# Performance work log

Hardware: AMD Instinct MI355X
Metric: run time of the kernel (lower is better)

The kernel has to match this reference:

```python
import jax, jax.numpy as jnp
import numpy as np

B, T, C = 4, 2048, 1024
H = 16
D = C // H  # head_dim = 64

def setup_inputs() -> dict:
    key = jax.random.key(0)
    k1, k2, k3 = jax.random.split(key, 3)
    x = jax.random.normal(k1, (B, T, C), dtype=jnp.float32)
    w_qkv = jax.random.normal(k2, (C, 3 * C), dtype=jnp.float32) * (1.0 / np.sqrt(C))
    w_proj = jax.random.normal(k3, (C, C), dtype=jnp.float32) * (1.0 / np.sqrt(C))
    return {"x": x, "w_qkv": w_qkv, "w_proj": w_proj}

def reference(x, w_qkv, w_proj):
    Bq, Tq, Cq = x.shape
    qkv = x @ w_qkv                                   # [B,T,3C]
    q, k, v = jnp.split(qkv, 3, axis=2)
    # [B,T,C] -> [B,H,T,D]
    q = q.reshape(Bq, Tq, H, D).transpose(0, 2, 1, 3)
    k = k.reshape(Bq, Tq, H, D).transpose(0, 2, 1, 3)
    v = v.reshape(Bq, Tq, H, D).transpose(0, 2, 1, 3)
    att = jnp.einsum('bhqd,bhkd->bhqk', q, k) / jnp.sqrt(jnp.float32(D))
    causal = jnp.tril(jnp.ones((Tq, Tq), dtype=bool))
    att = jnp.where(causal[None, None], att, jnp.float32(-jnp.inf))
    att = jax.nn.softmax(att, axis=-1)
    y = jnp.einsum('bhqk,bhkd->bhqd', att, v)         # [B,H,T,D]
    y = y.transpose(0, 2, 1, 3).reshape(Bq, Tq, Cq)
    return y @ w_proj
```

## Files before the change

kernel.cpp:

```cpp
#include <hip/hip_runtime.h>

typedef unsigned short u16;
typedef __attribute__((ext_vector_type(8))) short s16x8;
typedef __attribute__((ext_vector_type(4))) float f32x4;
typedef __attribute__((ext_vector_type(16))) float f32x16;

#define MFMA(a, b, c) __builtin_amdgcn_mfma_f32_16x16x32_bf16((a), (b), (c), 0, 0, 0)
#define MFMA32(a, b, c) __builtin_amdgcn_mfma_f32_32x32x16_bf16((a), (b), (c), 0, 0, 0)

#define LDS16(gp, lp)                                                          \
  __builtin_amdgcn_global_load_lds(                                            \
      (__attribute__((address_space(1))) void*)(gp),                           \
      (__attribute__((address_space(3))) void*)(lp), 16, 0, 0)

#if __has_builtin(__builtin_amdgcn_exp2f)
#define EXP2F(x) __builtin_amdgcn_exp2f(x)
#else
#define EXP2F(x) exp2f(x)
#endif
#if __has_builtin(__builtin_amdgcn_rcpf)
#define RCPF(x) __builtin_amdgcn_rcpf(x)
#else
#define RCPF(x) (1.0f / (x))
#endif

__device__ __forceinline__ u16 f2bf(float f) {
  unsigned u = __float_as_uint(f);
  u += 0x7fffu + ((u >> 16) & 1u);
  return (u16)(u >> 16);
}

__device__ __forceinline__ int cvtpk(float a, float b) {
  int r;
  asm("v_cvt_pk_bf16_f32 %0, %1, %2" : "=v"(r) : "v"(a), "v"(b));
  return r;
}

__global__ void cast_x_kernel(const float* __restrict__ in, u16* __restrict__ out) {
  const int idx = (blockIdx.x * 256 + threadIdx.x) * 4;
  const float4 v = *(const float4*)(in + idx);
  ushort4 o;
  o.x = f2bf(v.x); o.y = f2bf(v.y); o.z = f2bf(v.z); o.w = f2bf(v.w);
  *(ushort4*)(out + idx) = o;
}

__global__ void transpose_cast(const float* __restrict__ in, u16* __restrict__ out,
                               int Kd, int Nd) {
  __shared__ float t[64][65];
  const int tid = threadIdx.x;
  const int nb = blockIdx.x * 64, kb = blockIdx.y * 64;
#pragma unroll
  for (int it = 0; it < 4; it++) {
    const int flat = it * 1024 + tid * 4;
    const int rr = flat >> 6, cc = flat & 63;
    const float4 v = *(const float4*)(in + (size_t)(kb + rr) * Nd + nb + cc);
    t[rr][cc] = v.x; t[rr][cc + 1] = v.y; t[rr][cc + 2] = v.z; t[rr][cc + 3] = v.w;
  }
  __syncthreads();
#pragma unroll
  for (int it = 0; it < 4; it++) {
    const int flat = it * 1024 + tid * 4;
    const int rn = flat >> 6, ck = flat & 63;
    ushort4 o;
    o.x = f2bf(t[ck][rn]);     o.y = f2bf(t[ck + 1][rn]);
    o.z = f2bf(t[ck + 2][rn]); o.w = f2bf(t[ck + 3][rn]);
    *(ushort4*)(out + (size_t)(nb + rn) * Kd + kb + ck) = o;
  }
}

template <int EPI>
__global__ __launch_bounds__(256, 2)
void gemm128(const u16* __restrict__ A, const u16* __restrict__ Bt,
             float* __restrict__ Cout, int Ndim,
             u16* __restrict__ qp, u16* __restrict__ kp, u16* __restrict__ vp) {
  __shared__ alignas(16) u16 As[128 * 32];
  __shared__ alignas(16) u16 Bs[128 * 32];
  const int tid = threadIdx.x;
  const int wave = tid >> 6, lane = tid & 63;
  const int r = lane & 15, qq = lane >> 4;
  const int wm = (wave >> 1) * 64, wn = (wave & 1) * 64;
  const int gx = gridDim.x;
  const int nwg = gx * gridDim.y;
  const int bid = blockIdx.x + gx * blockIdx.y;
  const int swz = (bid & 7) * (nwg >> 3) + (bid >> 3);
  const int tn = (swz % gx) * 128, tm = (swz / gx) * 128;

  f32x4 acc[4][4];
#pragma unroll
  for (int i = 0; i < 4; i++)
#pragma unroll
    for (int j = 0; j < 4; j++) acc[i][j] = (f32x4){0.f, 0.f, 0.f, 0.f};

  const int c0 = tid, c1 = tid + 256;
  const u16* ga0 = A + (size_t)(tm + (c0 >> 2)) * 1024 + (c0 & 3) * 8;
  const u16* ga1 = A + (size_t)(tm + (c1 >> 2)) * 1024 + (c1 & 3) * 8;
  const u16* gb0 = Bt + (size_t)(tn + (c0 >> 2)) * 1024 + (c0 & 3) * 8;
  const u16* gb1 = Bt + (size_t)(tn + (c1 >> 2)) * 1024 + (c1 & 3) * 8;
  u16* la0 = As + c0 * 8; u16* la1 = As + c1 * 8;
  u16* lb0 = Bs + c0 * 8; u16* lb1 = Bs + c1 * 8;

  for (int k0 = 0; k0 < 1024; k0 += 32) {
    LDS16(ga0 + k0, la0);
    LDS16(ga1 + k0, la1);
    LDS16(gb0 + k0, lb0);
    LDS16(gb1 + k0, lb1);
    __syncthreads();
    s16x8 af[4], bfr[4];
#pragma unroll
    for (int f = 0; f < 4; f++)
      af[f] = *(const s16x8*)(As + (wm + f * 16 + r) * 32 + qq * 8);
#pragma unroll
    for (int f = 0; f < 4; f++)
      bfr[f] = *(const s16x8*)(Bs + (wn + f * 16 + r) * 32 + qq * 8);
    __builtin_amdgcn_s_setprio(1);
#pragma unroll
    for (int fm = 0; fm < 4; fm++)
#pragma unroll
      for (int fn = 0; fn < 4; fn++)
        acc[fm][fn] = MFMA(af[fm], bfr[fn], acc[fm][fn]);
    __builtin_amdgcn_s_setprio(0);
    __syncthreads();
  }

  if (EPI == 0) {
#pragma unroll
    for (int fm = 0; fm < 4; fm++) {
#pragma unroll
      for (int j2 = 0; j2 < 4; j2++) {
        const int mm = tm + wm + fm * 16 + qq * 4 + j2;
        const int bb = mm >> 11, tt = mm & 2047;
#pragma unroll
        for (int fn = 0; fn < 4; fn++) {
          const int n = tn + wn + fn * 16 + r;
          const u16 bv = f2bf(acc[fm][fn][j2]);
          const int which = n >> 10;
          const int hh = (n >> 6) & 15, dd = n & 63;
          const int bhh = bb * 16 + hh;
          if (which == 0)      qp[((size_t)bhh * 2048 + tt) * 64 + dd] = bv;
          else if (which == 1) kp[((size_t)bhh * 2048 + tt) * 64 + dd] = bv;
          else                 vp[((size_t)bhh * 64 + dd) * 2048 + tt] = bv;
        }
      }
    }
  } else {
#pragma unroll
    for (int fm = 0; fm < 4; fm++) {
#pragma unroll
      for (int j2 = 0; j2 < 4; j2++) {
        const int mm = tm + wm + fm * 16 + qq * 4 + j2;
#pragma unroll
        for (int fn = 0; fn < 4; fn++) {
          const int n = tn + wn + fn * 16 + r;
          Cout[(size_t)mm * Ndim + n] = acc[fm][fn][j2];
        }
      }
    }
  }
}

__global__ __launch_bounds__(256, 2)
void attn_fwd(const u16* __restrict__ qg, const u16* __restrict__ kg,
              const u16* __restrict__ vtg, u16* __restrict__ yg) {
  __shared__ alignas(16) u16 Kl[2][64 * 64];
  __shared__ alignas(16) u16 Vl[2][64 * 64];
  const int tid = threadIdx.x;
  const int w = tid >> 6, lane = tid & 63;
  const int q5 = lane & 31, hi = lane >> 5;
  const int bh = blockIdx.x;
  const int qi = (int)(gridDim.y - 1 - blockIdx.y);
  const int qb = qi * 128;
  const int qrow = qb + w * 32 + q5;
  const float C = 0.18033688011112042f;

  const u16* qbase = qg + ((size_t)bh * 2048 + qrow) * 64;
  s16x8 qf[4];
#pragma unroll
  for (int ks = 0; ks < 4; ks++)
    qf[ks] = *(const s16x8*)(qbase + ks * 16 + hi * 8);

  const int c0 = tid, c1 = tid + 256;
  const int r0 = c0 >> 3, s0 = (c0 & 7) ^ (r0 & 7);
  const int r1 = c1 >> 3, s1 = (c1 & 7) ^ (r1 & 7);
  const u16* kga = kg + ((size_t)bh * 2048 + r0) * 64 + s0 * 8;
  const u16* kgb = kg + ((size_t)bh * 2048 + r1) * 64 + s1 * 8;
  const u16* vga = vtg + ((size_t)bh * 64 + r0) * 2048 + s0 * 8;
  const u16* vgb = vtg + ((size_t)bh * 64 + r1) * 2048 + s1 * 8;

  f32x16 ya, yb;
#pragma unroll
  for (int r = 0; r < 16; r++) { ya[r] = 0.f; yb[r] = 0.f; }
  float m_run = -3.0e38f, l_run = 0.f;

  const int nt = qb / 64 + 2;

#define STAGE(b, t)                                               \
  do {                                                            \
    LDS16(kga + (size_t)(t) * 4096, Kl[b] + c0 * 8);              \
    LDS16(kgb + (size_t)(t) * 4096, Kl[b] + c1 * 8);              \
    LDS16(vga + (size_t)(t) * 64,   Vl[b] + c0 * 8);              \
    LDS16(vgb + (size_t)(t) * 64,   Vl[b] + c1 * 8);              \
  } while (0)

  STAGE(0, 0);
  __syncthreads();

  for (int t = 0; t < nt; t++) {
    const int buf = t & 1;
    if (t + 1 < nt) STAGE(buf ^ 1, t + 1);
    const int kv0 = t * 64;
    const u16* Kb = Kl[buf];
    const u16* Vb = Vl[buf];

    if (kv0 <= qb + w * 32 + 31) {
      f32x16 sa, sb;
#pragma unroll
      for (int r = 0; r < 16; r++) { sa[r] = 0.f; sb[r] = 0.f; }
      __builtin_amdgcn_s_setprio(1);
#pragma unroll
      for (int ks = 0; ks < 4; ks++) {
        const int slot = ((ks * 2 + hi) ^ (lane & 7)) * 8;
        const s16x8 ka  = *(const s16x8*)(Kb + q5 * 64 + slot);
        const s16x8 kb2 = *(const s16x8*)(Kb + (32 + q5) * 64 + slot);
        sa = MFMA32(ka, qf[ks], sa);
        sb = MFMA32(kb2, qf[ks], sb);
      }
      __builtin_amdgcn_s_setprio(0);

      s16x8 va[4], vb2[4];
#pragma unroll
      for (int ks4 = 0; ks4 < 4; ks4++) {
        const int sv = ((ks4 * 2 + hi) ^ (lane & 7)) * 8;
        va[ks4]  = *(const s16x8*)(Vb + q5 * 64 + sv);
        vb2[ks4] = *(const s16x8*)(Vb + (32 + q5) * 64 + sv);
      }

      if (kv0 + 63 > qb + w * 32) {
#pragma unroll
        for (int r = 0; r < 16; r++) {
          const int kl = kv0 + (r & 3) + 8 * (r >> 2) + 4 * hi;
          if (kl > qrow)      sa[r] = -3.0e38f;
          if (kl + 32 > qrow) sb[r] = -3.0e38f;
        }
      }

      float mx0 = -3.0e38f, mx1 = -3.0e38f, mx2 = -3.0e38f, mx3 = -3.0e38f;
#pragma unroll
      for (int r = 0; r < 16; r += 4) {
        mx0 = fmaxf(mx0, fmaxf(sa[r], sb[r]));
        mx1 = fmaxf(mx1, fmaxf(sa[r + 1], sb[r + 1]));
        mx2 = fmaxf(mx2, fmaxf(sa[r + 2], sb[r + 2]));
        mx3 = fmaxf(mx3, fmaxf(sa[r + 3], sb[r + 3]));
      }
      float mx = fmaxf(fmaxf(mx0, mx1), fmaxf(mx2, mx3));
      mx = fmaxf(mx, __shfl_xor(mx, 32));
      const float mxs = mx * C;

      if (!__all(mxs - m_run <= 8.0f)) {
        const float m2 = fmaxf(m_run, mxs);
        const float alpha = EXP2F(m_run - m2);
        m_run = m2;
        l_run *= alpha;
#pragma unroll
        for (int r = 0; r < 16; r++) { ya[r] *= alpha; yb[r] *= alpha; }
      }

      const float nm2 = -m_run;
      float ls0 = 0.f, ls1 = 0.f, ls2 = 0.f, ls3 = 0.f;
#pragma unroll
      for (int r = 0; r < 16; r += 4) {
        float p;
        p = EXP2F(fmaf(sa[r], C, nm2));     sa[r] = p;     ls0 += p;
        p = EXP2F(fmaf(sa[r + 1], C, nm2)); sa[r + 1] = p; ls1 += p;
        p = EXP2F(fmaf(sa[r + 2], C, nm2)); sa[r + 2] = p; ls2 += p;
        p = EXP2F(fmaf(sa[r + 3], C, nm2)); sa[r + 3] = p; ls3 += p;
        p = EXP2F(fmaf(sb[r], C, nm2));     sb[r] = p;     ls0 += p;
        p = EXP2F(fmaf(sb[r + 1], C, nm2)); sb[r + 1] = p; ls1 += p;
        p = EXP2F(fmaf(sb[r + 2], C, nm2)); sb[r + 2] = p; ls2 += p;
        p = EXP2F(fmaf(sb[r + 3], C, nm2)); sb[r + 3] = p; ls3 += p;
      }
      float ls = (ls0 + ls1) + (ls2 + ls3);
      ls += __shfl_xor(ls, 32);
      l_run += ls;

      s16x8 bfrag[4];
#pragma unroll
      for (int kb = 0; kb < 2; kb++) {
        const f32x16* pv = kb ? &sb : &sa;
        int wv[8], xv[8];
#pragma unroll
        for (int i = 0; i < 8; i++) wv[i] = cvtpk((*pv)[2 * i], (*pv)[2 * i + 1]);
#pragma unroll
        for (int i = 0; i < 8; i++) xv[i] = __shfl_xor(wv[i], 32);
        union { int4 i4; s16x8 s8; } u0, u1;
        u0.i4 = hi ? make_int4(xv[2], xv[3], wv[2], wv[3])
                   : make_int4(wv[0], wv[1], xv[0], xv[1]);
        u1.i4 = hi ? make_int4(xv[6], xv[7], wv[6], wv[7])
                   : make_int4(wv[4], wv[5], xv[4], xv[5]);
        bfrag[kb * 2]     = u0.s8;
        bfrag[kb * 2 + 1] = u1.s8;
      }

      __builtin_amdgcn_s_setprio(1);
#pragma unroll
      for (int ks4 = 0; ks4 < 4; ks4++) {
        ya = MFMA32(va[ks4], bfrag[ks4], ya);
        yb = MFMA32(vb2[ks4], bfrag[ks4], yb);
      }
      __builtin_amdgcn_s_setprio(0);
    }
    __syncthreads();
  }
#undef STAGE

  const float linv = RCPF(l_run);
  const int b = bh >> 4, h = bh & 15;
  u16* yrow = yg + ((size_t)b * 2048 + qrow) * 1024 + h * 64;
#pragma unroll
  for (int dt = 0; dt < 2; dt++) {
    const f32x16* Y = dt ? &yb : &ya;
#pragma unroll
    for (int p2 = 0; p2 < 8; p2++) {
      const int pk = cvtpk((*Y)[2 * p2] * linv, (*Y)[2 * p2 + 1] * linv);
      const int d0 = dt * 32 + (p2 >> 1) * 8 + hi * 4 + (p2 & 1) * 2;
      *reinterpret_cast<int*>(yrow + d0) = pk;
    }
  }
}

extern "C" void kernel_launch(void* const* d_in, const int* in_sizes, int n_in,
                              void* d_out, int out_size, void* d_ws, size_t ws_size,
                              hipStream_t stream) {
  const float* x = (const float*)d_in[0];
  const float* wqkv = (const float*)d_in[1];
  const float* wproj = (const float*)d_in[2];
  float* out = (float*)d_out;

  char* ws = (char*)d_ws;
  u16* xb     = (u16*)(ws);
  u16* wqkvT  = (u16*)(ws + 16777216);
  u16* wprojT = (u16*)(ws + 23068672);
  u16* qw     = (u16*)(ws + 25165824);
  u16* kw     = (u16*)(ws + 41943040);
  u16* vtw    = (u16*)(ws + 58720256);
  u16* yw     = (u16*)(ws + 75497472);
  (void)in_sizes; (void)n_in; (void)out_size; (void)ws_size;

  cast_x_kernel<<<8192, 256, 0, stream>>>(x, xb);
  transpose_cast<<<dim3(48, 16), 256, 0, stream>>>(wqkv, wqkvT, 1024, 3072);
  transpose_cast<<<dim3(16, 16), 256, 0, stream>>>(wproj, wprojT, 1024, 1024);
  gemm128<0><<<dim3(24, 64), 256, 0, stream>>>(xb, wqkvT, nullptr, 3072, qw, kw, vtw);
  attn_fwd<<<dim3(64, 16), 256, 0, stream>>>(qw, kw, vtw, yw);
  gemm128<1><<<dim3(8, 64), 256, 0, stream>>>(yw, wprojT, out, 1024,
                                              nullptr, nullptr, nullptr);
}
```

Baseline: 269.8 us.

## Pipeline GEMM with 4-stage LDS ring and 256x128 tiles using 512 threads

Replaces the single-buffered 128x128 GEMM with a 256x128 tile computed by 8 waves. The K-loop now streams into a 4-slot LDS ring, issuing global-to-LDS loads three stages ahead and using vmcnt waits plus one barrier per step. This hides global load latency and removes the second barrier per iteration. In exchange it uses more LDS per block (96KB) and adds a k-major LDS layout that may cause bank conflicts.

```diff
diff --git a/kernel.cpp b/kernel.cpp
--- a/kernel.cpp
+++ b/kernel.cpp
@@ -12,6 +12,8 @@
   __builtin_amdgcn_global_load_lds(                                            \
       (__attribute__((address_space(1))) void*)(gp),                           \
       (__attribute__((address_space(3))) void*)(lp), 16, 0, 0)
+
+#define WAITVM(n) asm volatile("s_waitcnt vmcnt(" #n ")" ::: "memory")
 
 #if __has_builtin(__builtin_amdgcn_exp2f)
 #define EXP2F(x) __builtin_amdgcn_exp2f(x)
@@ -69,21 +71,20 @@
 }
 
 template <int EPI>
-__global__ __launch_bounds__(256, 2)
-void gemm128(const u16* __restrict__ A, const u16* __restrict__ Bt,
+__global__ __launch_bounds__(512, 2)
+void gemm256(const u16* __restrict__ A, const u16* __restrict__ Bt,
              float* __restrict__ Cout, int Ndim,
              u16* __restrict__ qp, u16* __restrict__ kp, u16* __restrict__ vp) {
-  __shared__ alignas(16) u16 As[128 * 32];
-  __shared__ alignas(16) u16 Bs[128 * 32];
+  __shared__ alignas(16) u16 L[4 * 12288];
   const int tid = threadIdx.x;
-  const int wave = tid >> 6, lane = tid & 63;
+  const int lane = tid & 63, wid = tid >> 6;
   const int r = lane & 15, qq = lane >> 4;
-  const int wm = (wave >> 1) * 64, wn = (wave & 1) * 64;
+  const int wr = wid >> 1, wc = wid & 1;
   const int gx = gridDim.x;
   const int nwg = gx * gridDim.y;
   const int bid = blockIdx.x + gx * blockIdx.y;
   const int swz = (bid & 7) * (nwg >> 3) + (bid >> 3);
-  const int tn = (swz % gx) * 128, tm = (swz / gx) * 128;
+  const int tn = (swz % gx) * 128, tm = (swz / gx) * 256;
 
   f32x4 acc[4][4];
 #pragma unroll
@@ -91,47 +92,70 @@
 #pragma unroll
     for (int j = 0; j < 4; j++) acc[i][j] = (f32x4){0.f, 0.f, 0.f, 0.f};
 
-  const int c0 = tid, c1 = tid + 256;
-  const u16* ga0 = A + (size_t)(tm + (c0 >> 2)) * 1024 + (c0 & 3) * 8;
-  const u16* ga1 = A + (size_t)(tm + (c1 >> 2)) * 1024 + (c1 & 3) * 8;
-  const u16* gb0 = Bt + (size_t)(tn + (c0 >> 2)) * 1024 + (c0 & 3) * 8;
-  const u16* gb1 = Bt + (size_t)(tn + (c1 >> 2)) * 1024 + (c1 & 3) * 8;
-  u16* la0 = As + c0 * 8; u16* la1 = As + c1 * 8;
-  u16* lb0 = Bs + c0 * 8; u16* lb1 = Bs + c1 * 8;
-
-  for (int k0 = 0; k0 < 1024; k0 += 32) {
-    LDS16(ga0 + k0, la0);
-    LDS16(ga1 + k0, la1);
-    LDS16(gb0 + k0, lb0);
-    LDS16(gb1 + k0, lb1);
-    __syncthreads();
-    s16x8 af[4], bfr[4];
-#pragma unroll
-    for (int f = 0; f < 4; f++)
-      af[f] = *(const s16x8*)(As + (wm + f * 16 + r) * 32 + qq * 8);
-#pragma unroll
-    for (int f = 0; f < 4; f++)
-      bfr[f] = *(const s16x8*)(Bs + (wn + f * 16 + r) * 32 + qq * 8);
-    __builtin_amdgcn_s_setprio(1);
-#pragma unroll
-    for (int fm = 0; fm < 4; fm++)
-#pragma unroll
-      for (int fn = 0; fn < 4; fn++)
-        acc[fm][fn] = MFMA(af[fm], bfr[fn], acc[fm][fn]);
-    __builtin_amdgcn_s_setprio(0);
-    __syncthreads();
-  }
+  const u16* gA = A + (size_t)(tm + (tid & 255)) * 1024 + (tid >> 8) * 8;
+  const u16* gB = Bt + (size_t)(tn + (tid & 127)) * 1024 + (tid >> 7) * 8;
+  const int la0 = tid * 8, la1 = (tid + 512) * 8, lb0 = 8192 + tid * 8;
+
+#define GSTAGE(b, t)                                                \
+  do {                                                              \
+    const u16* ga_ = gA + (t) * 32;                                 \
+    u16* lp_ = L + (b) * 12288;                                     \
+    LDS16(ga_, lp_ + la0);                                          \
+    LDS16(ga_ + 16, lp_ + la1);                                     \
+    LDS16(gB + (t) * 32, lp_ + lb0);                                \
+  } while (0)
+
+  const int arow = wr * 64 + r, brow = wc * 64 + r;
+  const int aoff = qq * 2048 + arow * 8;
+  const int boff = 8192 + qq * 1024 + brow * 8;
+
+#define GCOMPUTE(b)                                                 \
+  do {                                                              \
+    const u16* lp_ = L + (b) * 12288;                               \
+    s16x8 af[4], bfv[4];                                            \
+    _Pragma("unroll")                                               \
+    for (int f = 0; f < 4; f++)                                     \
+      af[f] = *(const s16x8*)(lp_ + aoff + f * 128);                \
+    _Pragma("unroll")                                               \
+    for (int f = 0; f < 4; f++)                                     \
+      bfv[f] = *(const s16x8*)(lp_ + boff + f * 128);               \
+    __builtin_amdgcn_s_setprio(1);                                  \
+    _Pragma("unroll")                                               \
+    for (int fm = 0; fm < 4; fm++)                                  \
+      _Pragma("unroll")                                             \
+      for (int fn = 0; fn < 4; fn++)                                \
+        acc[fm][fn] = MFMA(af[fm], bfv[fn], acc[fm][fn]);           \
+    __builtin_amdgcn_s_setprio(0);                                  \
+  } while (0)
+
+  GSTAGE(0, 0);
+  GSTAGE(1, 1);
+  GSTAGE(2, 2);
+  for (int kt = 0; kt < 30; kt++) {
+    WAITVM(6);
+    __builtin_amdgcn_s_barrier();
+    if (kt < 29) GSTAGE((kt + 3) & 3, kt + 3);
+    GCOMPUTE(kt & 3);
+  }
+  WAITVM(3);
+  __builtin_amdgcn_s_barrier();
+  GCOMPUTE(2);
+  WAITVM(0);
+  __builtin_amdgcn_s_barrier();
+  GCOMPUTE(3);
+#undef GSTAGE
+#undef GCOMPUTE
 
   if (EPI == 0) {
 #pragma unroll
     for (int fm = 0; fm < 4; fm++) {
 #pragma unroll
       for (int j2 = 0; j2 < 4; j2++) {
-        const int mm = tm + wm + fm * 16 + qq * 4 + j2;
+        const int mm = tm + wr * 64 + fm * 16 + qq * 4 + j2;
         const int bb = mm >> 11, tt = mm & 2047;
 #pragma unroll
         for (int fn = 0; fn < 4; fn++) {
-          const int n = tn + wn + fn * 16 + r;
+          const int n = tn + wc * 64 + fn * 16 + r;
           const u16 bv = f2bf(acc[fm][fn][j2]);
           const int which = n >> 10;
           const int hh = (n >> 6) & 15, dd = n & 63;
@@ -147,10 +171,10 @@
     for (int fm = 0; fm < 4; fm++) {
 #pragma unroll
       for (int j2 = 0; j2 < 4; j2++) {
-        const int mm = tm + wm + fm * 16 + qq * 4 + j2;
+        const int mm = tm + wr * 64 + fm * 16 + qq * 4 + j2;
 #pragma unroll
         for (int fn = 0; fn < 4; fn++) {
-          const int n = tn + wn + fn * 16 + r;
+          const int n = tn + wc * 64 + fn * 16 + r;
           Cout[(size_t)mm * Ndim + n] = acc[fm][fn][j2];
         }
       }
@@ -348,8 +372,8 @@
   cast_x_kernel<<<8192, 256, 0, stream>>>(x, xb);
   transpose_cast<<<dim3(48, 16), 256, 0, stream>>>(wqkv, wqkvT, 1024, 3072);
   transpose_cast<<<dim3(16, 16), 256, 0, stream>>>(wproj, wprojT, 1024, 1024);
-  gemm128<0><<<dim3(24, 64), 256, 0, stream>>>(xb, wqkvT, nullptr, 3072, qw, kw, vtw);
+  gemm256<0><<<dim3(24, 32), 512, 0, stream>>>(xb, wqkvT, nullptr, 3072, qw, kw, vtw);
   attn_fwd<<<dim3(64, 16), 256, 0, stream>>>(qw, kw, vtw, yw);
-  gemm128<1><<<dim3(8, 64), 256, 0, stream>>>(yw, wprojT, out, 1024,
+  gemm256<1><<<dim3(8, 32), 512, 0, stream>>>(yw, wprojT, out, 1024,
                                               nullptr, nullptr, nullptr);
 }
```

After: 320.6 us. 18.8% more time.
